# Kernel tuning notes

Hardware: AMD Instinct MI355X
Metric: run time of the kernel (lower is better)

## Reference

```python
import jax, jax.numpy as jnp
import numpy as np

D_MODEL = 1024
N_HEAD = 16
D_HEAD = D_MODEL // N_HEAD


def setup_inputs() -> dict:
    key = jax.random.key(0)
    k_x, k_wqkv, k_bqkv, k_wp, k_bp = jax.random.split(key, 5)
    B, T = 2, 2048
    bound = 1.0 / np.sqrt(D_MODEL)
    return {
        "x": jax.random.normal(k_x, (B, T, D_MODEL), dtype=jnp.float32),
        "w_qkv": jax.random.uniform(k_wqkv, (D_MODEL, 3 * D_MODEL), jnp.float32, -bound, bound),
        "b_qkv": jax.random.uniform(k_bqkv, (3 * D_MODEL,), jnp.float32, -bound, bound),
        "w_proj": jax.random.uniform(k_wp, (D_MODEL, D_MODEL), jnp.float32, -bound, bound),
        "b_proj": jax.random.uniform(k_bp, (D_MODEL,), jnp.float32, -bound, bound),
    }


def reference(x, w_qkv, b_qkv, w_proj, b_proj):
    B, T, C = x.shape
    qkv = x @ w_qkv + b_qkv                       # [B,T,3C]
    qkv = qkv.reshape(B, T, 3, N_HEAD, D_HEAD)
    qkv = jnp.transpose(qkv, (2, 0, 3, 1, 4))      # [3,B,H,T,dh]
    q, k, v = qkv[0], qkv[1], qkv[2]
    scale = np.sqrt(D_HEAD).astype(np.float32)
    attn = jnp.einsum("bhqd,bhkd->bhqk", q, k) / scale  # [B,H,T,T]
    causal = jnp.tril(jnp.ones((T, T), dtype=bool))
    attn = jnp.where(causal, attn, -jnp.inf)
    attn = jax.nn.softmax(attn, axis=-1)
    out = jnp.einsum("bhqk,bhkd->bhqd", attn, v)   # [B,H,T,dh]
    out = jnp.transpose(out, (0, 2, 1, 3)).reshape(B, T, C)
    return out @ w_proj + b_proj
```

## Files before the change

### kernel.cpp

```cpp
#include <hip/hip_runtime.h>
#include <hip/hip_bf16.h>
#include <math.h>

constexpr int Bb   = 2;
constexpr int T    = 2048;
constexpr int C    = 1024;
constexpr int H    = 16;
constexpr int M    = Bb * T;
constexpr int NQKV = 3 * C;

typedef __attribute__((ext_vector_type(8))) short bf16x8;
typedef __attribute__((ext_vector_type(4))) float f32x4;

__device__ inline short f2bf(float f) {
    __hip_bfloat16 h = __float2bfloat16(f);
    return *reinterpret_cast<short*>(&h);
}

#if __has_builtin(__builtin_amdgcn_exp2f)
#define EXP2(x) __builtin_amdgcn_exp2f(x)
#else
#define EXP2(x) exp2f(x)
#endif

#define GLOBAL_AS __attribute__((address_space(1)))
#define LDS_AS    __attribute__((address_space(3)))

__device__ __forceinline__ void gload_lds16(const short* g, short* s) {
    __builtin_amdgcn_global_load_lds((const GLOBAL_AS void*)g, (LDS_AS void*)s, 16, 0, 0);
}

__global__ __launch_bounds__(256)
void prep_all(const float* __restrict__ x, short* __restrict__ xb,
              const float* __restrict__ w_qkv, short* __restrict__ wqkvt,
              const float* __restrict__ w_proj, short* __restrict__ wprojt)
{
    __shared__ float tile[32][33];
    const int blk = blockIdx.x;
    const int tid = threadIdx.x;

    if (blk < 4096) {
        const int i = blk * 1024 + tid * 4;
        const float4 v = *(const float4*)(x + i);
        short4 s;
        s.x = f2bf(v.x); s.y = f2bf(v.y); s.z = f2bf(v.z); s.w = f2bf(v.w);
        *(short4*)(xb + i) = s;
        return;
    }

    const bool isqkv = (blk < 7168);
    const int bidx = isqkv ? (blk - 4096) : (blk - 7168);
    const int nblk = isqkv ? 96 : 32;
    const int N    = isqkv ? NQKV : C;
    const float* W = isqkv ? w_qkv : w_proj;
    short* Wt      = isqkv ? wqkvt : wprojt;

    const int n0 = (bidx % nblk) * 32, k0 = (bidx / nblk) * 32;
    const int tx = tid & 31, ty = tid >> 5;
#pragma unroll
    for (int i = 0; i < 32; i += 8)
        tile[ty + i][tx] = W[(size_t)(k0 + ty + i) * N + n0 + tx];
    __syncthreads();
#pragma unroll
    for (int i = 0; i < 32; i += 8)
        Wt[(size_t)(n0 + ty + i) * C + k0 + tx] = f2bf(tile[tx][ty + i]);
}

__global__ __launch_bounds__(256)
void gemm_mfma(const short* __restrict__ A, const short* __restrict__ Bt,
               const float* __restrict__ bias, short* __restrict__ outp,
               int Ndim, int Kdim)
{
    __shared__ __align__(16) short As[2 * 128 * 32];
    __shared__ __align__(16) short Bs[2 * 128 * 32];

    const int tid = threadIdx.x;
    const int w   = tid >> 6;
    const int l   = tid & 63;
    const int lk  = l & 15;
    const int lq  = l >> 4;

    const int gx  = gridDim.x;
    const int nwg = gx * gridDim.y;
    const int cpx = nwg >> 3;
    const int bid = blockIdx.y * gx + blockIdx.x;
    const int swz = (bid & 7) * cpx + (bid >> 3);
    const int m0  = (swz / gx) * 128;
    const int n0  = (swz % gx) * 128;

    const int mw  = (w >> 1) * 64, nw = (w & 1) * 64;

    const int srow = w * 16 + (l >> 2);
    const int scol = (l & 3) * 8;

    const short* agp0 = A  + (size_t)(m0 + srow)      * Kdim + scol;
    const short* agp1 = A  + (size_t)(m0 + 64 + srow) * Kdim + scol;
    const short* bgp0 = Bt + (size_t)(n0 + srow)      * Kdim + scol;
    const short* bgp1 = Bt + (size_t)(n0 + 64 + srow) * Kdim + scol;

    short* ad0 = &As[w * 512];
    short* ad1 = &As[2048 + w * 512];
    short* bd0 = &Bs[w * 512];
    short* bd1 = &Bs[2048 + w * 512];

    f32x4 acc[4][4];
#pragma unroll
    for (int i = 0; i < 4; ++i)
#pragma unroll
        for (int j = 0; j < 4; ++j) acc[i][j] = (f32x4){0.f, 0.f, 0.f, 0.f};

    gload_lds16(agp0, ad0);
    gload_lds16(agp1, ad1);
    gload_lds16(bgp0, bd0);
    gload_lds16(bgp1, bd1);
    __syncthreads();

    int cur = 0;
    for (int k0 = 0; k0 < Kdim; k0 += 32) {
        const int coff = cur ? 4096 : 0;

        bf16x8 af[4], bfr[4];
#pragma unroll
        for (int mt = 0; mt < 4; ++mt)
            af[mt] = *(const bf16x8*)&As[coff + (mw + mt * 16 + lk) * 32 + lq * 8];
#pragma unroll
        for (int nt = 0; nt < 4; ++nt)
            bfr[nt] = *(const bf16x8*)&Bs[coff + (nw + nt * 16 + lk) * 32 + lq * 8];

        if (k0 + 32 < Kdim) {
            const int noff = cur ? 0 : 4096;
            gload_lds16(agp0 + k0 + 32, ad0 + noff);
            gload_lds16(agp1 + k0 + 32, ad1 + noff);
            gload_lds16(bgp0 + k0 + 32, bd0 + noff);
            gload_lds16(bgp1 + k0 + 32, bd1 + noff);
        }

#pragma unroll
        for (int mt = 0; mt < 4; ++mt)
#pragma unroll
            for (int nt = 0; nt < 4; ++nt)
                acc[mt][nt] = __builtin_amdgcn_mfma_f32_16x16x32_bf16(bfr[nt], af[mt], acc[mt][nt], 0, 0, 0);

        __syncthreads();
        cur ^= 1;
    }

    float4 bv[4];
#pragma unroll
    for (int nt = 0; nt < 4; ++nt)
        bv[nt] = *(const float4*)(bias + n0 + nw + nt * 16 + lq * 4);
#pragma unroll
    for (int mt = 0; mt < 4; ++mt) {
        short* rowp = outp + (size_t)(m0 + mw + mt * 16 + lk) * Ndim + n0 + nw + lq * 4;
#pragma unroll
        for (int nt = 0; nt < 4; ++nt) {
            short4 pk;
            pk.x = f2bf(acc[mt][nt][0] + bv[nt].x);
            pk.y = f2bf(acc[mt][nt][1] + bv[nt].y);
            pk.z = f2bf(acc[mt][nt][2] + bv[nt].z);
            pk.w = f2bf(acc[mt][nt][3] + bv[nt].w);
            *(short4*)(rowp + nt * 16) = pk;
        }
    }
}

__global__ __launch_bounds__(256)
void gemm_mfma_proj(const short* __restrict__ A, const short* __restrict__ Bt,
                    const float* __restrict__ bias, float* __restrict__ outp,
                    int Ndim, int Kdim)
{
    __shared__ __align__(16) short As[2 * 64 * 32];
    __shared__ __align__(16) short Bs[2 * 128 * 32];

    const int tid = threadIdx.x;
    const int w   = tid >> 6;
    const int l   = tid & 63;
    const int lk  = l & 15;
    const int lq  = l >> 4;

    const int gx  = gridDim.x;
    const int nwg = gx * gridDim.y;
    const int cpx = nwg >> 3;
    const int bid = blockIdx.y * gx + blockIdx.x;
    const int swz = (bid & 7) * cpx + (bid >> 3);
    const int m0  = (swz / gx) * 64;
    const int n0  = (swz % gx) * 128;

    const int mw  = (w & 1) * 32, nw = (w >> 1) * 64;

    const int srow = w * 16 + (l >> 2);
    const int scol = (l & 3) * 8;

    const short* agp  = A  + (size_t)(m0 + srow)      * Kdim + scol;
    const short* bgp0 = Bt + (size_t)(n0 + srow)      * Kdim + scol;
    const short* bgp1 = Bt + (size_t)(n0 + 64 + srow) * Kdim + scol;

    short* ad  = &As[w * 512];
    short* bd0 = &Bs[w * 512];
    short* bd1 = &Bs[2048 + w * 512];

    f32x4 acc[2][4];
#pragma unroll
    for (int i = 0; i < 2; ++i)
#pragma unroll
        for (int j = 0; j < 4; ++j) acc[i][j] = (f32x4){0.f, 0.f, 0.f, 0.f};

    gload_lds16(agp,  ad);
    gload_lds16(bgp0, bd0);
    gload_lds16(bgp1, bd1);
    __syncthreads();

    int cur = 0;
    for (int k0 = 0; k0 < Kdim; k0 += 32) {
        const int coffA = cur ? 2048 : 0;
        const int coffB = cur ? 4096 : 0;

        bf16x8 af[2], bfr[4];
#pragma unroll
        for (int mt = 0; mt < 2; ++mt)
            af[mt] = *(const bf16x8*)&As[coffA + (mw + mt * 16 + lk) * 32 + lq * 8];
#pragma unroll
        for (int nt = 0; nt < 4; ++nt)
            bfr[nt] = *(const bf16x8*)&Bs[coffB + (nw + nt * 16 + lk) * 32 + lq * 8];

        if (k0 + 32 < Kdim) {
            const int noffA = cur ? 0 : 2048;
            const int noffB = cur ? 0 : 4096;
            gload_lds16(agp  + k0 + 32, ad  + noffA);
            gload_lds16(bgp0 + k0 + 32, bd0 + noffB);
            gload_lds16(bgp1 + k0 + 32, bd1 + noffB);
        }

#pragma unroll
        for (int mt = 0; mt < 2; ++mt)
#pragma unroll
            for (int nt = 0; nt < 4; ++nt)
                acc[mt][nt] = __builtin_amdgcn_mfma_f32_16x16x32_bf16(bfr[nt], af[mt], acc[mt][nt], 0, 0, 0);

        __syncthreads();
        cur ^= 1;
    }

    float4 bv[4];
#pragma unroll
    for (int nt = 0; nt < 4; ++nt)
        bv[nt] = *(const float4*)(bias + n0 + nw + nt * 16 + lq * 4);
#pragma unroll
    for (int mt = 0; mt < 2; ++mt) {
        float* rowp = outp + (size_t)(m0 + mw + mt * 16 + lk) * Ndim + n0 + nw + lq * 4;
#pragma unroll
        for (int nt = 0; nt < 4; ++nt) {
            float4 v;
            v.x = acc[mt][nt][0] + bv[nt].x;
            v.y = acc[mt][nt][1] + bv[nt].y;
            v.z = acc[mt][nt][2] + bv[nt].z;
            v.w = acc[mt][nt][3] + bv[nt].w;
            *(float4*)(rowp + nt * 16) = v;
        }
    }
}

constexpr int LDV = 136;
constexpr float SC = 0.18033688f;

__global__ __launch_bounds__(512, 4)
void attn_mfma(const short* __restrict__ qkv, short* __restrict__ att)
{
    __shared__ __align__(16) short Ks[2][128 * 64];
    __shared__ __align__(16) short Vt[2][64 * LDV];

    const int idx = blockIdx.x;
    const int xcd = idx & 7;
    const int j   = idx >> 3;
    const int bh  = xcd * 4 + (j & 3);
    const int s   = j >> 2;
    const int qt  = (s < 8) ? s : (23 - s);
    const int b   = bh >> 4;
    const int h   = bh & 15;
    const int qbase = qt * 128;

    const int tid = threadIdx.x;
    const int w   = tid >> 6;
    const int l   = tid & 63;
    const int lk  = l & 15;
    const int lq  = l >> 4;

    const short* base = qkv + (size_t)b * T * 3072 + h * 64;

    const int q_abs = qbase + w * 16 + lk;
    const short* qp = base + (size_t)q_abs * 3072 + lq * 8;
    const bf16x8 qf0 = *(const bf16x8*)qp;
    const bf16x8 qf1 = *(const bf16x8*)(qp + 32);

    f32x4 acc_o[4];
#pragma unroll
    for (int dt = 0; dt < 4; ++dt) acc_o[dt] = (f32x4){0.f, 0.f, 0.f, 0.f};
    float m_run = -INFINITY;
    float l_run = 0.f;

    const int krow   = l >> 3;
    const int kcolsw = 8 * ((l & 7) ^ (l >> 3));
    const int swz    = lk & 7;

    const int kg   = tid & 31;
    const int vd0  = ((tid >> 5) & 7) * 8;
    const int pcol = ((kg & 24) | ((kg & 3) << 1) | ((kg >> 2) & 1)) * 4;

    const int nkt = qt + 1;

    bf16x8 vv[4];

    if (w < 4) {
#pragma unroll
        for (int rr = 0; rr < 4; ++rr) {
            const int g = w * 32 + rr * 8;
            gload_lds16(base + 1024 + (size_t)(g + krow) * 3072 + kcolsw, &Ks[0][g * 64]);
        }
    } else {
        const short* vp = base + 2048 + (size_t)(kg * 4) * 3072 + vd0;
#pragma unroll
        for (int kk = 0; kk < 4; ++kk)
            vv[kk] = *(const bf16x8*)(vp + (size_t)kk * 3072);
#pragma unroll
        for (int d = 0; d < 8; ++d) {
            short4 pk;
            pk.x = vv[0][d]; pk.y = vv[1][d]; pk.z = vv[2][d]; pk.w = vv[3][d];
            *(short4*)&Vt[0][(vd0 + d) * LDV + pcol] = pk;
        }
    }
    __syncthreads();

#pragma unroll 1
    for (int it = 0; it < nkt; ++it) {
        const int j0  = it * 128;
        const int buf = it & 1;
        const int nb  = buf ^ 1;

        if (it + 1 < nkt) {
            const int j1 = j0 + 128;
            if (w < 4) {
#pragma unroll
                for (int rr = 0; rr < 4; ++rr) {
                    const int g = w * 32 + rr * 8;
                    gload_lds16(base + 1024 + (size_t)(j1 + g + krow) * 3072 + kcolsw,
                                &Ks[nb][g * 64]);
                }
            } else {
                const short* vp = base + 2048 + (size_t)(j1 + kg * 4) * 3072 + vd0;
#pragma unroll
                for (int kk = 0; kk < 4; ++kk)
                    vv[kk] = *(const bf16x8*)(vp + (size_t)kk * 3072);
            }
        }

        f32x4 s4[8];
#pragma unroll
        for (int kt = 0; kt < 8; ++kt) {
            const int row = kt * 16 + lk;
            const bf16x8 kf0 = *(const bf16x8*)&Ks[buf][row * 64 + 8 * (lq ^ swz)];
            const bf16x8 kf1 = *(const bf16x8*)&Ks[buf][row * 64 + 8 * ((lq + 4) ^ swz)];
            f32x4 a = (f32x4){0.f, 0.f, 0.f, 0.f};
            a = __builtin_amdgcn_mfma_f32_16x16x32_bf16(kf0, qf0, a, 0, 0, 0);
            a = __builtin_amdgcn_mfma_f32_16x16x32_bf16(kf1, qf1, a, 0, 0, 0);
            s4[kt] = a;
        }

        if (it == nkt - 1) {
#pragma unroll
            for (int kt = 0; kt < 8; ++kt)
#pragma unroll
                for (int r = 0; r < 4; ++r)
                    if (j0 + kt * 16 + lq * 4 + r > q_abs) s4[kt][r] = -1e30f;
        }

        float mx = s4[0][0];
#pragma unroll
        for (int kt = 0; kt < 8; ++kt)
#pragma unroll
            for (int r = 0; r < 4; ++r) mx = fmaxf(mx, s4[kt][r]);
        mx = fmaxf(mx, __shfl_xor(mx, 16));
        mx = fmaxf(mx, __shfl_xor(mx, 32));
        const float mn   = fmaxf(m_run, mx);
        const float corr = EXP2((m_run - mn) * SC);
        m_run = mn;
        const float nmc = -mn * SC;
#pragma unroll
        for (int kt = 0; kt < 8; ++kt)
#pragma unroll
            for (int r = 0; r < 4; ++r)
                s4[kt][r] = EXP2(fmaf(s4[kt][r], SC, nmc));
        float ps = 0.f;
#pragma unroll
        for (int kt = 0; kt < 8; ++kt)
            ps += ((s4[kt][0] + s4[kt][1]) + (s4[kt][2] + s4[kt][3]));
        ps += __shfl_xor(ps, 16);
        ps += __shfl_xor(ps, 32);
        l_run = l_run * corr + ps;

        unsigned int d0[8], d1[8];
#pragma unroll
        for (int kt = 0; kt < 8; ++kt) {
            d0[kt] = (unsigned int)(unsigned short)f2bf(s4[kt][0])
                   | ((unsigned int)(unsigned short)f2bf(s4[kt][1]) << 16);
            d1[kt] = (unsigned int)(unsigned short)f2bf(s4[kt][2])
                   | ((unsigned int)(unsigned short)f2bf(s4[kt][3]) << 16);
        }

#pragma unroll
        for (int dt = 0; dt < 4; ++dt)
#pragma unroll
            for (int r = 0; r < 4; ++r) acc_o[dt][r] *= corr;

#pragma unroll
        for (int kc = 0; kc < 4; ++kc) {
            union { unsigned int u[4]; bf16x8 v; } up;
            up.u[0] = d0[kc * 2];
            up.u[1] = d1[kc * 2];
            up.u[2] = d0[kc * 2 + 1];
            up.u[3] = d1[kc * 2 + 1];
            const bf16x8 pf = up.v;
#pragma unroll
            for (int dt = 0; dt < 4; ++dt) {
                const bf16x8 vf = *(const bf16x8*)&Vt[buf][(dt * 16 + lk) * LDV + kc * 32 + lq * 8];
                acc_o[dt] = __builtin_amdgcn_mfma_f32_16x16x32_bf16(vf, pf, acc_o[dt], 0, 0, 0);
            }
        }

        if (it + 1 < nkt && w >= 4) {
#pragma unroll
            for (int d = 0; d < 8; ++d) {
                short4 pk;
                pk.x = vv[0][d]; pk.y = vv[1][d]; pk.z = vv[2][d]; pk.w = vv[3][d];
                *(short4*)&Vt[nb][(vd0 + d) * LDV + pcol] = pk;
            }
        }

        __syncthreads();
    }

    const float inv = 1.f / l_run;
    short* op = att + ((size_t)(b * T + q_abs)) * 1024 + h * 64;
#pragma unroll
    for (int dt = 0; dt < 4; ++dt) {
        short4 pk;
        pk.x = f2bf(acc_o[dt][0] * inv);
        pk.y = f2bf(acc_o[dt][1] * inv);
        pk.z = f2bf(acc_o[dt][2] * inv);
        pk.w = f2bf(acc_o[dt][3] * inv);
        *(short4*)(op + dt * 16 + lq * 4) = pk;
    }
}

extern "C" void kernel_launch(void* const* d_in, const int* in_sizes, int n_in,
                              void* d_out, int out_size, void* d_ws, size_t ws_size,
                              hipStream_t stream)
{
    const float* x      = (const float*)d_in[0];
    const float* w_qkv  = (const float*)d_in[1];
    const float* b_qkv  = (const float*)d_in[2];
    const float* w_proj = (const float*)d_in[3];
    const float* b_proj = (const float*)d_in[4];
    float* out = (float*)d_out;

    short* xb     = (short*)d_ws;
    short* wqkvt  = xb     + (size_t)M * C;
    short* wprojt = wqkvt  + (size_t)NQKV * C;
    short* qkvb   = wprojt + (size_t)C * C;
    short* attb   = qkvb   + (size_t)M * NQKV;

    prep_all<<<8192, 256, 0, stream>>>(x, xb, w_qkv, wqkvt, w_proj, wprojt);
    gemm_mfma<<<dim3(NQKV / 128, M / 128), 256, 0, stream>>>(xb, wqkvt, b_qkv, qkvb, NQKV, C);
    attn_mfma<<<512, 512, 0, stream>>>(qkvb, attb);
    gemm_mfma_proj<<<dim3(C / 128, M / 64), 256, 0, stream>>>(attb, wprojt, b_proj, out, C, C);
}
```

Before: 177.6 us.

## Pair causal q-tiles per block and spread K/V staging across all waves

The attention kernel now launches 256 blocks, and each block handles two query tiles (s and 15-s), so every block does the same amount of causal work. K and V tile loading is now split evenly across all 8 waves instead of 4 doing K and 4 doing V, and V is transposed with a packed two-row shuffle. The loop also skips the rescale when no row max grows and raises wave priority around the MFMA sections. Fewer blocks and lower launch bounds may reduce occupancy and latency hiding, and the extra branches add divergence checks.

```diff
diff --git a/kernel.cpp b/kernel.cpp
--- a/kernel.cpp
+++ b/kernel.cpp
@@ -263,7 +263,7 @@
 constexpr int LDV = 136;
 constexpr float SC = 0.18033688f;
 
-__global__ __launch_bounds__(512, 4)
+__global__ __launch_bounds__(512, 2)
 void attn_mfma(const short* __restrict__ qkv, short* __restrict__ att)
 {
     __shared__ __align__(16) short Ks[2][128 * 64];
@@ -271,13 +271,11 @@
 
     const int idx = blockIdx.x;
     const int xcd = idx & 7;
-    const int j   = idx >> 3;
-    const int bh  = xcd * 4 + (j & 3);
-    const int s   = j >> 2;
-    const int qt  = (s < 8) ? s : (23 - s);
+    const int r   = idx >> 3;
+    const int bh  = xcd * 4 + (r & 3);
+    const int s   = r >> 2;
     const int b   = bh >> 4;
     const int h   = bh & 15;
-    const int qbase = qt * 128;
 
     const int tid = threadIdx.x;
     const int w   = tid >> 6;
@@ -287,167 +285,189 @@
 
     const short* base = qkv + (size_t)b * T * 3072 + h * 64;
 
-    const int q_abs = qbase + w * 16 + lk;
-    const short* qp = base + (size_t)q_abs * 3072 + lq * 8;
-    const bf16x8 qf0 = *(const bf16x8*)qp;
-    const bf16x8 qf1 = *(const bf16x8*)(qp + 32);
-
-    f32x4 acc_o[4];
-#pragma unroll
-    for (int dt = 0; dt < 4; ++dt) acc_o[dt] = (f32x4){0.f, 0.f, 0.f, 0.f};
-    float m_run = -INFINITY;
-    float l_run = 0.f;
-
-    const int krow   = l >> 3;
     const int kcolsw = 8 * ((l & 7) ^ (l >> 3));
-    const int swz    = lk & 7;
-
-    const int kg   = tid & 31;
-    const int vd0  = ((tid >> 5) & 7) * 8;
-    const int pcol = ((kg & 24) | ((kg & 3) << 1) | ((kg >> 2) & 1)) * 4;
-
-    const int nkt = qt + 1;
-
-    bf16x8 vv[4];
-
-    if (w < 4) {
-#pragma unroll
-        for (int rr = 0; rr < 4; ++rr) {
-            const int g = w * 32 + rr * 8;
-            gload_lds16(base + 1024 + (size_t)(g + krow) * 3072 + kcolsw, &Ks[0][g * 64]);
-        }
-    } else {
-        const short* vp = base + 2048 + (size_t)(kg * 4) * 3072 + vd0;
-#pragma unroll
-        for (int kk = 0; kk < 4; ++kk)
-            vv[kk] = *(const bf16x8*)(vp + (size_t)kk * 3072);
-#pragma unroll
-        for (int d = 0; d < 8; ++d) {
+    const int swz    = lk & 15 & 7;
+
+    const int k2  = tid & 63;
+    const int vd0 = (tid >> 6) * 8;
+    const int kk   = (2 * k2) & 31;
+    const int vcol = ((2 * k2) >> 5) * 32 + ((kk >> 2) & 3) * 8
+                   + ((kk >> 4) & 1) * 4 + (kk & 3);
+
+    uint4 va, vb;
+
+    for (int pi = 0; pi < 2; ++pi) {
+        const int qt    = pi ? (15 - s) : s;
+        const int qbase = qt * 128;
+        const int nkt   = qt + 1;
+
+        const int q_abs = qbase + w * 16 + lk;
+        const short* qp = base + (size_t)q_abs * 3072 + lq * 8;
+        const bf16x8 qf0 = *(const bf16x8*)qp;
+        const bf16x8 qf1 = *(const bf16x8*)(qp + 32);
+
+        f32x4 acc_o[4];
+#pragma unroll
+        for (int dt = 0; dt < 4; ++dt) acc_o[dt] = (f32x4){0.f, 0.f, 0.f, 0.f};
+        float m_run = -INFINITY;
+        float l_run = 0.f;
+
+        __syncthreads();
+#pragma unroll
+        for (int rr = 0; rr < 2; ++rr) {
+            const int rowbase = rr * 64 + w * 8;
+            gload_lds16(base + 1024 + (size_t)(rowbase + (l >> 3)) * 3072 + kcolsw,
+                        &Ks[0][rowbase * 64]);
+        }
+        {
+            const short* vp = base + 2048 + (size_t)(2 * k2) * 3072 + vd0;
+            va = *(const uint4*)vp;
+            vb = *(const uint4*)(vp + 3072);
+            const unsigned int Aa[4] = {va.x, va.y, va.z, va.w};
+            const unsigned int Bbv[4] = {vb.x, vb.y, vb.z, vb.w};
+#pragma unroll
+            for (int p = 0; p < 4; ++p) {
+                const unsigned int ue = (Aa[p] & 0xffffu) | (Bbv[p] << 16);
+                const unsigned int uo = (Aa[p] >> 16) | (Bbv[p] & 0xffff0000u);
+                *(unsigned int*)&Vt[0][(vd0 + 2 * p)     * LDV + vcol] = ue;
+                *(unsigned int*)&Vt[0][(vd0 + 2 * p + 1) * LDV + vcol] = uo;
+            }
+        }
+        __syncthreads();
+
+#pragma unroll 1
+        for (int it = 0; it < nkt; ++it) {
+            const int j0  = it * 128;
+            const int buf = it & 1;
+            const int nb  = buf ^ 1;
+
+            if (it + 1 < nkt) {
+                const int j1 = j0 + 128;
+#pragma unroll
+                for (int rr = 0; rr < 2; ++rr) {
+                    const int rowbase = rr * 64 + w * 8;
+                    gload_lds16(base + 1024 + (size_t)(j1 + rowbase + (l >> 3)) * 3072 + kcolsw,
+                                &Ks[nb][rowbase * 64]);
+                }
+                const short* vp = base + 2048 + (size_t)(j1 + 2 * k2) * 3072 + vd0;
+                va = *(const uint4*)vp;
+                vb = *(const uint4*)(vp + 3072);
+            }
+
+            f32x4 s4[8];
+            __builtin_amdgcn_s_setprio(1);
+#pragma unroll
+            for (int kt = 0; kt < 8; ++kt) {
+                const int row = kt * 16 + lk;
+                const bf16x8 kf0 = *(const bf16x8*)&Ks[buf][row * 64 + 8 * (lq ^ swz)];
+                const bf16x8 kf1 = *(const bf16x8*)&Ks[buf][row * 64 + 8 * ((lq + 4) ^ swz)];
+                f32x4 a = (f32x4){0.f, 0.f, 0.f, 0.f};
+                a = __builtin_amdgcn_mfma_f32_16x16x32_bf16(kf0, qf0, a, 0, 0, 0);
+                a = __builtin_amdgcn_mfma_f32_16x16x32_bf16(kf1, qf1, a, 0, 0, 0);
+                s4[kt] = a;
+            }
+            __builtin_amdgcn_s_setprio(0);
+
+            if (it == nkt - 1) {
+#pragma unroll
+                for (int kt = 0; kt < 8; ++kt)
+#pragma unroll
+                    for (int r2 = 0; r2 < 4; ++r2)
+                        if (j0 + kt * 16 + lq * 4 + r2 > q_abs) s4[kt][r2] = -1e30f;
+            }
+
+            float tm[8];
+#pragma unroll
+            for (int kt = 0; kt < 8; ++kt)
+                tm[kt] = fmaxf(fmaxf(s4[kt][0], s4[kt][1]), fmaxf(s4[kt][2], s4[kt][3]));
+            float mx = fmaxf(fmaxf(fmaxf(tm[0], tm[1]), fmaxf(tm[2], tm[3])),
+                             fmaxf(fmaxf(tm[4], tm[5]), fmaxf(tm[6], tm[7])));
+            mx = fmaxf(mx, __shfl_xor(mx, 16));
+            mx = fmaxf(mx, __shfl_xor(mx, 32));
+
+            const bool grow = __any(mx > m_run);
+            float corr = 1.f;
+            if (grow) {
+                const float mn = fmaxf(m_run, mx);
+                corr = EXP2((m_run - mn) * SC);
+                m_run = mn;
+            }
+            const float nmc = -m_run * SC;
+#pragma unroll
+            for (int kt = 0; kt < 8; ++kt)
+#pragma unroll
+                for (int r2 = 0; r2 < 4; ++r2)
+                    s4[kt][r2] = EXP2(fmaf(s4[kt][r2], SC, nmc));
+
+            float ts[8];
+#pragma unroll
+            for (int kt = 0; kt < 8; ++kt)
+                ts[kt] = (s4[kt][0] + s4[kt][1]) + (s4[kt][2] + s4[kt][3]);
+            float ps = ((ts[0] + ts[1]) + (ts[2] + ts[3]))
+                     + ((ts[4] + ts[5]) + (ts[6] + ts[7]));
+            ps += __shfl_xor(ps, 16);
+            ps += __shfl_xor(ps, 32);
+            l_run = grow ? (l_run * corr + ps) : (l_run + ps);
+
+            unsigned int d0[8], d1[8];
+#pragma unroll
+            for (int kt = 0; kt < 8; ++kt) {
+                d0[kt] = (unsigned int)(unsigned short)f2bf(s4[kt][0])
+                       | ((unsigned int)(unsigned short)f2bf(s4[kt][1]) << 16);
+                d1[kt] = (unsigned int)(unsigned short)f2bf(s4[kt][2])
+                       | ((unsigned int)(unsigned short)f2bf(s4[kt][3]) << 16);
+            }
+
+            if (grow) {
+#pragma unroll
+                for (int dt = 0; dt < 4; ++dt)
+#pragma unroll
+                    for (int r2 = 0; r2 < 4; ++r2) acc_o[dt][r2] *= corr;
+            }
+
+            __builtin_amdgcn_s_setprio(1);
+#pragma unroll
+            for (int kc = 0; kc < 4; ++kc) {
+                union { unsigned int u[4]; bf16x8 v; } up;
+                up.u[0] = d0[kc * 2];
+                up.u[1] = d1[kc * 2];
+                up.u[2] = d0[kc * 2 + 1];
+                up.u[3] = d1[kc * 2 + 1];
+                const bf16x8 pf = up.v;
+#pragma unroll
+                for (int dt = 0; dt < 4; ++dt) {
+                    const bf16x8 vf = *(const bf16x8*)&Vt[buf][(dt * 16 + lk) * LDV + kc * 32 + lq * 8];
+                    acc_o[dt] = __builtin_amdgcn_mfma_f32_16x16x32_bf16(vf, pf, acc_o[dt], 0, 0, 0);
+                }
+            }
+            __builtin_amdgcn_s_setprio(0);
+
+            if (it + 1 < nkt) {
+                const unsigned int Aa[4] = {va.x, va.y, va.z, va.w};
+                const unsigned int Bbv[4] = {vb.x, vb.y, vb.z, vb.w};
+#pragma unroll
+                for (int p = 0; p < 4; ++p) {
+                    const unsigned int ue = (Aa[p] & 0xffffu) | (Bbv[p] << 16);
+                    const unsigned int uo = (Aa[p] >> 16) | (Bbv[p] & 0xffff0000u);
+                    *(unsigned int*)&Vt[nb][(vd0 + 2 * p)     * LDV + vcol] = ue;
+                    *(unsigned int*)&Vt[nb][(vd0 + 2 * p + 1) * LDV + vcol] = uo;
+                }
+            }
+
+            __syncthreads();
+        }
+
+        const float inv = 1.f / l_run;
+        short* op = att + ((size_t)(b * T + q_abs)) * 1024 + h * 64;
+#pragma unroll
+        for (int dt = 0; dt < 4; ++dt) {
             short4 pk;
-            pk.x = vv[0][d]; pk.y = vv[1][d]; pk.z = vv[2][d]; pk.w = vv[3][d];
-            *(short4*)&Vt[0][(vd0 + d) * LDV + pcol] = pk;
-        }
-    }
-    __syncthreads();
-
-#pragma unroll 1
-    for (int it = 0; it < nkt; ++it) {
-        const int j0  = it * 128;
-        const int buf = it & 1;
-        const int nb  = buf ^ 1;
-
-        if (it + 1 < nkt) {
-            const int j1 = j0 + 128;
-            if (w < 4) {
-#pragma unroll
-                for (int rr = 0; rr < 4; ++rr) {
-                    const int g = w * 32 + rr * 8;
-                    gload_lds16(base + 1024 + (size_t)(j1 + g + krow) * 3072 + kcolsw,
-                                &Ks[nb][g * 64]);
-                }
-            } else {
-                const short* vp = base + 2048 + (size_t)(j1 + kg * 4) * 3072 + vd0;
-#pragma unroll
-                for (int kk = 0; kk < 4; ++kk)
-                    vv[kk] = *(const bf16x8*)(vp + (size_t)kk * 3072);
-            }
-        }
-
-        f32x4 s4[8];
-#pragma unroll
-        for (int kt = 0; kt < 8; ++kt) {
-            const int row = kt * 16 + lk;
-            const bf16x8 kf0 = *(const bf16x8*)&Ks[buf][row * 64 + 8 * (lq ^ swz)];
-            const bf16x8 kf1 = *(const bf16x8*)&Ks[buf][row * 64 + 8 * ((lq + 4) ^ swz)];
-            f32x4 a = (f32x4){0.f, 0.f, 0.f, 0.f};
-            a = __builtin_amdgcn_mfma_f32_16x16x32_bf16(kf0, qf0, a, 0, 0, 0);
-            a = __builtin_amdgcn_mfma_f32_16x16x32_bf16(kf1, qf1, a, 0, 0, 0);
-            s4[kt] = a;
-        }
-
-        if (it == nkt - 1) {
-#pragma unroll
-            for (int kt = 0; kt < 8; ++kt)
-#pragma unroll
-                for (int r = 0; r < 4; ++r)
-                    if (j0 + kt * 16 + lq * 4 + r > q_abs) s4[kt][r] = -1e30f;
-        }
-
-        float mx = s4[0][0];
-#pragma unroll
-        for (int kt = 0; kt < 8; ++kt)
-#pragma unroll
-            for (int r = 0; r < 4; ++r) mx = fmaxf(mx, s4[kt][r]);
-        mx = fmaxf(mx, __shfl_xor(mx, 16));
-        mx = fmaxf(mx, __shfl_xor(mx, 32));
-        const float mn   = fmaxf(m_run, mx);
-        const float corr = EXP2((m_run - mn) * SC);
-        m_run = mn;
-        const float nmc = -mn * SC;
-#pragma unroll
-        for (int kt = 0; kt < 8; ++kt)
-#pragma unroll
-            for (int r = 0; r < 4; ++r)
-                s4[kt][r] = EXP2(fmaf(s4[kt][r], SC, nmc));
-        float ps = 0.f;
-#pragma unroll
-        for (int kt = 0; kt < 8; ++kt)
-            ps += ((s4[kt][0] + s4[kt][1]) + (s4[kt][2] + s4[kt][3]));
-        ps += __shfl_xor(ps, 16);
-        ps += __shfl_xor(ps, 32);
-        l_run = l_run * corr + ps;
-
-        unsigned int d0[8], d1[8];
-#pragma unroll
-        for (int kt = 0; kt < 8; ++kt) {
-            d0[kt] = (unsigned int)(unsigned short)f2bf(s4[kt][0])
-                   | ((unsigned int)(unsigned short)f2bf(s4[kt][1]) << 16);
-            d1[kt] = (unsigned int)(unsigned short)f2bf(s4[kt][2])
-                   | ((unsigned int)(unsigned short)f2bf(s4[kt][3]) << 16);
-        }
-
-#pragma unroll
-        for (int dt = 0; dt < 4; ++dt)
-#pragma unroll
-            for (int r = 0; r < 4; ++r) acc_o[dt][r] *= corr;
-
-#pragma unroll
-        for (int kc = 0; kc < 4; ++kc) {
-            union { unsigned int u[4]; bf16x8 v; } up;
-            up.u[0] = d0[kc * 2];
-            up.u[1] = d1[kc * 2];
-            up.u[2] = d0[kc * 2 + 1];
-            up.u[3] = d1[kc * 2 + 1];
-            const bf16x8 pf = up.v;
-#pragma unroll
-            for (int dt = 0; dt < 4; ++dt) {
-                const bf16x8 vf = *(const bf16x8*)&Vt[buf][(dt * 16 + lk) * LDV + kc * 32 + lq * 8];
-                acc_o[dt] = __builtin_amdgcn_mfma_f32_16x16x32_bf16(vf, pf, acc_o[dt], 0, 0, 0);
-            }
-        }
-
-        if (it + 1 < nkt && w >= 4) {
-#pragma unroll
-            for (int d = 0; d < 8; ++d) {
-                short4 pk;
-                pk.x = vv[0][d]; pk.y = vv[1][d]; pk.z = vv[2][d]; pk.w = vv[3][d];
-                *(short4*)&Vt[nb][(vd0 + d) * LDV + pcol] = pk;
-            }
-        }
-
-        __syncthreads();
-    }
-
-    const float inv = 1.f / l_run;
-    short* op = att + ((size_t)(b * T + q_abs)) * 1024 + h * 64;
-#pragma unroll
-    for (int dt = 0; dt < 4; ++dt) {
-        short4 pk;
-        pk.x = f2bf(acc_o[dt][0] * inv);
-        pk.y = f2bf(acc_o[dt][1] * inv);
-        pk.z = f2bf(acc_o[dt][2] * inv);
-        pk.w = f2bf(acc_o[dt][3] * inv);
-        *(short4*)(op + dt * 16 + lq * 4) = pk;
+            pk.x = f2bf(acc_o[dt][0] * inv);
+            pk.y = f2bf(acc_o[dt][1] * inv);
+            pk.z = f2bf(acc_o[dt][2] * inv);
+            pk.w = f2bf(acc_o[dt][3] * inv);
+            *(short4*)(op + dt * 16 + lq * 4) = pk;
+        }
     }
 }
 
@@ -470,6 +490,6 @@
 
     prep_all<<<8192, 256, 0, stream>>>(x, xb, w_qkv, wqkvt, w_proj, wprojt);
     gemm_mfma<<<dim3(NQKV / 128, M / 128), 256, 0, stream>>>(xb, wqkvt, b_qkv, qkvb, NQKV, C);
-    attn_mfma<<<512, 512, 0, stream>>>(qkvb, attb);
+    attn_mfma<<<256, 512, 0, stream>>>(qkvb, attb);
     gemm_mfma_proj<<<dim3(C / 128, M / 64), 256, 0, stream>>>(attb, wprojt, b_proj, out, C, C);
 }
```

Result: slower. 188.0 us (+5.8%).
